# Kernel tuning notes

Measured on AMD Instinct MI355X. Metric: run time of the kernel, lower is better.

The kernel has to match this reference:

```python
import jax, jax.numpy as jnp
import numpy as np

EPS = 1e-5  # BatchNorm eps
N_NODES, N_EDGES, F = 100000, 600000, 128


def setup_inputs() -> dict:
    key = jax.random.key(0)
    ks = jax.random.split(key, 16)
    inp = {
        "node_representations": jax.random.normal(ks[0], (N_NODES, F), jnp.float32),
        "edges": jax.random.randint(ks[1], (2, N_EDGES), 0, N_NODES, jnp.int64 if jax.config.jax_enable_x64 else jnp.int32),
        "edge_weights": jax.random.uniform(ks[2], (N_EDGES,), jnp.float32),
        # preprocess FFN: BatchNorm1d(F) [eval mode] + Linear(F, F) + GELU
        "pre_bn_gamma": jax.random.normal(ks[3], (F,), jnp.float32) * 0.1 + 1.0,
        "pre_bn_beta": jax.random.normal(ks[4], (F,), jnp.float32) * 0.1,
        "pre_bn_mean": jax.random.normal(ks[5], (F,), jnp.float32) * 0.1,
        "pre_bn_var": jax.random.uniform(ks[6], (F,), jnp.float32) * 0.5 + 0.5,
        "pre_w": jax.random.normal(ks[7], (F, F), jnp.float32) / np.sqrt(F),
        "pre_b": jnp.zeros((F,), jnp.float32),
        # update FFN: BatchNorm1d(2F) [eval mode] + Linear(2F, F) + GELU
        "upd_bn_gamma": jax.random.normal(ks[8], (2 * F,), jnp.float32) * 0.1 + 1.0,
        "upd_bn_beta": jax.random.normal(ks[9], (2 * F,), jnp.float32) * 0.1,
        "upd_bn_mean": jax.random.normal(ks[10], (2 * F,), jnp.float32) * 0.1,
        "upd_bn_var": jax.random.uniform(ks[11], (2 * F,), jnp.float32) * 0.5 + 0.5,
        "upd_w": jax.random.normal(ks[12], (2 * F, F), jnp.float32) / np.sqrt(2 * F),
        "upd_b": jnp.zeros((F,), jnp.float32),
    }
    return inp


def _bn_eval(x, gamma, beta, mean, var):
    return (x - mean) * (gamma / jnp.sqrt(var + EPS)) + beta


def reference(node_representations, edges, edge_weights,
              pre_bn_gamma, pre_bn_beta, pre_bn_mean, pre_bn_var, pre_w, pre_b,
              upd_bn_gamma, upd_bn_beta, upd_bn_mean, upd_bn_var, upd_w, upd_b):
    n_nodes, f = node_representations.shape
    node_idx, nbr_idx = edges[0], edges[1]
    # gather neighbour features: [E, F]
    x = node_representations[nbr_idx]
    # preprocess FFN (BN eval, dropout=identity in eval, linear, gelu)
    x = _bn_eval(x, pre_bn_gamma, pre_bn_beta, pre_bn_mean, pre_bn_var)
    x = jax.nn.gelu(x @ pre_w + pre_b, approximate=False)
    x = x * edge_weights[:, None]
    # mean aggregation (replicates torch.unique-on-expanded-indices counter = degree * F)
    agg = jax.ops.segment_sum(x, node_idx, num_segments=n_nodes)
    deg = jax.ops.segment_sum(jnp.ones_like(edge_weights), node_idx, num_segments=n_nodes)
    counter = (deg * f)[:, None]
    agg = jnp.where(counter > 0, agg / jnp.where(counter > 0, counter, 1.0), 0.0)
    # concat combine + update FFN
    emb = jnp.concatenate([node_representations, agg], axis=-1)
    emb = _bn_eval(emb, upd_bn_gamma, upd_bn_beta, upd_bn_mean, upd_bn_var)
    emb = jax.nn.gelu(emb @ upd_w + upd_b, approximate=False)
    return emb
```

## Files before the change

### kernel.cpp

```cpp
#include <hip/hip_runtime.h>
#include <math.h>

#define F 128
#define TWO_F 256
#define BN_EPS 1e-5f
#define PAD_W1 136
#define PAD_W2 264

typedef unsigned short ushort_t;
typedef unsigned char uchar_t;
typedef __attribute__((ext_vector_type(8))) short bfrag;
typedef __attribute__((ext_vector_type(4))) float ffrag;
typedef __attribute__((ext_vector_type(2))) float floatx2;

__device__ __forceinline__ float gelu_exact(float x) {
    return 0.5f * x * (1.0f + erff(x * 0.70710678118654752f));
}
__device__ __forceinline__ ushort_t f2bf(float x) {
    unsigned int u = __float_as_uint(x);
    u = (u + 0x7FFFu + ((u >> 16) & 1u)) >> 16;
    return (ushort_t)u;
}
__device__ __forceinline__ unsigned int pk2(float a, float b) {
    return (unsigned int)f2bf(a) | ((unsigned int)f2bf(b) << 16);
}

__device__ __forceinline__ void fma4_fp8(float* acc, unsigned int d, float w) {
    floatx2 lo = __builtin_amdgcn_cvt_pk_f32_fp8(d, false);
    floatx2 hi = __builtin_amdgcn_cvt_pk_f32_fp8(d, true);
    acc[0] = fmaf(w, lo.x, acc[0]);
    acc[1] = fmaf(w, lo.y, acc[1]);
    acc[2] = fmaf(w, hi.x, acc[2]);
    acc[3] = fmaf(w, hi.y, acc[3]);
}
__device__ __forceinline__ void fma16_fp8(float* acc, uint4 a, float w) {
    fma4_fp8(acc + 0,  a.x, w); fma4_fp8(acc + 4,  a.y, w);
    fma4_fp8(acc + 8,  a.z, w); fma4_fp8(acc + 12, a.w, w);
}

__global__ __launch_bounds__(256) void prep(
    const float* __restrict__ pre_w, const float* __restrict__ pre_b,
    const float* __restrict__ g1, const float* __restrict__ be1,
    const float* __restrict__ m1, const float* __restrict__ v1,
    const float* __restrict__ upd_w, const float* __restrict__ upd_b,
    const float* __restrict__ g2, const float* __restrict__ be2,
    const float* __restrict__ m2, const float* __restrict__ v2,
    ushort_t* __restrict__ W1T, ushort_t* __restrict__ W2T,
    float* __restrict__ b1f, float* __restrict__ b2f,
    const float* __restrict__ nodes, ushort_t* __restrict__ NB, int convB, int nNodes,
    const int* __restrict__ edges, int* __restrict__ counts, int* __restrict__ rankb,
    int nEdges, int histBlocks) {
    const int t = threadIdx.x;
    if (blockIdx.x == 0) {
        __shared__ float t1[F], t2[TWO_F];
        if (t < F) {
            float s = g1[t] * rsqrtf(v1[t] + BN_EPS);
            t1[t] = be1[t] - m1[t] * s;
        }
        {
            float s = g2[t] * rsqrtf(v2[t] + BN_EPS);
            t2[t] = be2[t] - m2[t] * s;
        }
        __syncthreads();
        if (t < F) {
            float acc = pre_b[t];
            #pragma unroll 4
            for (int k = 0; k < F; ++k) acc = fmaf(t1[k], pre_w[k * F + t], acc);
            b1f[t] = acc;
        } else {
            int j = t - F;
            float acc = upd_b[j];
            #pragma unroll 4
            for (int k = 0; k < TWO_F; ++k) acc = fmaf(t2[k], upd_w[k * F + j], acc);
            b2f[j] = acc;
        }
    } else if (blockIdx.x <= 128) {
        int idx = (blockIdx.x - 1) * 256 + t;
        if (idx < F * F) {
            int k = idx & (F - 1), n = idx >> 7;
            float s = g1[k] * rsqrtf(v1[k] + BN_EPS);
            W1T[idx] = f2bf(s * pre_w[k * F + n]);
        }
        {
            int k = idx & (TWO_F - 1), n = idx >> 8;
            float s = g2[k] * rsqrtf(v2[k] + BN_EPS);
            W2T[idx] = f2bf(s * upd_w[k * F + n]);
        }
    } else if (blockIdx.x <= 128 + convB) {
        int cb = blockIdx.x - 129;
        long long idx = (long long)cb * 4096 + t * 16;
        if (idx < (long long)nNodes * F) {
            const float4* s = reinterpret_cast<const float4*>(nodes + idx);
            float4 f0 = s[0], f1 = s[1], f2 = s[2], f3 = s[3];
            uint4 o0, o1;
            o0.x = pk2(f0.x, f0.y); o0.y = pk2(f0.z, f0.w);
            o0.z = pk2(f1.x, f1.y); o0.w = pk2(f1.z, f1.w);
            o1.x = pk2(f2.x, f2.y); o1.y = pk2(f2.z, f2.w);
            o1.z = pk2(f3.x, f3.y); o1.w = pk2(f3.z, f3.w);
            uint4* d = reinterpret_cast<uint4*>(NB + idx);
            d[0] = o0; d[1] = o1;
        }
    } else {
        int b = blockIdx.x - 129 - convB;
        for (int i = b * 256 + t; i < nEdges; i += histBlocks * 256) {
            int rk = atomicAdd(&counts[edges[i]], 1);
            rankb[i] = rk;
        }
    }
}

__global__ __launch_bounds__(1024) void scan_pass1(const int* __restrict__ counts,
                                                   int* __restrict__ offsets,
                                                   int* __restrict__ blocksums, int n) {
    __shared__ int sb[1024];
    const int t = threadIdx.x;
    int idx = blockIdx.x * 1024 + t;
    int v = (idx < n) ? counts[idx] : 0;
    sb[t] = v;
    __syncthreads();
    for (int off = 1; off < 1024; off <<= 1) {
        int x = (t >= off) ? sb[t - off] : 0;
        __syncthreads();
        sb[t] += x;
        __syncthreads();
    }
    if (idx < n) offsets[idx + 1] = sb[t];
    if (t == 1023) blocksums[blockIdx.x] = sb[t];
}

__global__ __launch_bounds__(1024) void scan_pass3(const int* __restrict__ counts,
                                                   int* __restrict__ offsets,
                                                   const int* __restrict__ blocksums,
                                                   int* __restrict__ cursor, int n) {
    __shared__ int sb[1024];
    const int t = threadIdx.x;
    sb[t] = (t < blockIdx.x) ? blocksums[t] : 0;
    __syncthreads();
    #pragma unroll
    for (int off = 512; off > 0; off >>= 1) {
        if (t < off) sb[t] += sb[t + off];
        __syncthreads();
    }
    int base = sb[0];
    int idx = blockIdx.x * 1024 + t;
    if (idx < n) {
        int incl = offsets[idx + 1] + base;
        offsets[idx + 1] = incl;
        cursor[idx] = incl - counts[idx];
    }
    if (blockIdx.x == 0 && t == 0) offsets[0] = 0;
}

__global__ __launch_bounds__(256) void gemm1_fill(
    const ushort_t* __restrict__ NB, const ushort_t* __restrict__ W1T,
    const float* __restrict__ b1f, uchar_t* __restrict__ G8, int nNodes,
    const int* __restrict__ edges, const float* __restrict__ ew,
    const int* __restrict__ offsets, const int* __restrict__ rankb,
    int2* __restrict__ csr, int nEdges,
    int gemmBlocks, int fillBlocks, int nTiles) {
    __shared__ ushort_t Wl[F * PAD_W1];
    __shared__ float bsm[F];
    __shared__ uchar_t bounce[4][16 * F];
    const int t = threadIdx.x;

    if (blockIdx.x >= gemmBlocks) {
        int b = blockIdx.x - gemmBlocks;
        for (int e = b * 256 + t; e < nEdges; e += fillBlocks * 256) {
            int dst = edges[e];
            int pos = offsets[dst] + rankb[e];
            csr[pos] = make_int2(edges[nEdges + e], __float_as_int(ew[e]));
        }
        return;
    }

    for (int j = t; j < 2048; j += 256) {
        int feat = j >> 4, kc = j & 15;
        *reinterpret_cast<uint4*>(Wl + feat * PAD_W1 + kc * 8) =
            reinterpret_cast<const uint4*>(W1T)[j];
    }
    if (t < F) bsm[t] = b1f[t];
    __syncthreads();

    const int lane = t & 63, w = t >> 6;
    const int m = lane & 15, quad = lane >> 4;
    const int rr = lane >> 2, cc = (lane & 3) * 32;

    for (int tile = blockIdx.x; tile < nTiles; tile += gemmBlocks) {
        const int tb = tile * 64;
        int arow = tb + w * 16 + m;
        if (arow >= nNodes) arow = 0;
        const ushort_t* ap = NB + (size_t)arow * F + quad * 8;

        bfrag a[4];
        #pragma unroll
        for (int kk = 0; kk < 4; ++kk)
            a[kk] = *reinterpret_cast<const bfrag*>(ap + kk * 32);

        ffrag acc[8];
        #pragma unroll
        for (int c = 0; c < 8; ++c) acc[c] = (ffrag){0.f, 0.f, 0.f, 0.f};

        #pragma unroll
        for (int kk = 0; kk < 4; ++kk) {
            int k0 = kk * 32 + quad * 8;
            #pragma unroll
            for (int c = 0; c < 8; ++c) {
                bfrag b = *reinterpret_cast<const bfrag*>(Wl + (c * 16 + m) * PAD_W1 + k0);
                acc[c] = __builtin_amdgcn_mfma_f32_16x16x32_bf16(a[kk], b, acc[c], 0, 0, 0);
            }
        }

        #pragma unroll
        for (int c = 0; c < 8; ++c) {
            float bj = bsm[c * 16 + m];
            #pragma unroll
            for (int i = 0; i < 4; ++i) {
                float v = gelu_exact(acc[c][i] + bj);
                int pkd = __builtin_amdgcn_cvt_pk_fp8_f32(v, v, 0, false);
                bounce[w][(quad * 4 + i) * F + c * 16 + m] = (uchar_t)(pkd & 0xFF);
            }
        }
        uint4 d0 = *reinterpret_cast<const uint4*>(&bounce[w][rr * F + cc]);
        uint4 d1 = *reinterpret_cast<const uint4*>(&bounce[w][rr * F + cc + 16]);
        int gr = tb + w * 16 + rr;
        if (gr < nNodes) {
            *reinterpret_cast<uint4*>(G8 + (size_t)gr * F + cc) = d0;
            *reinterpret_cast<uint4*>(G8 + (size_t)gr * F + cc + 16) = d1;
        }
    }
}

__global__ __launch_bounds__(256) void gather_agg(
    const uchar_t* __restrict__ G8, const int* __restrict__ offsets,
    const int2* __restrict__ csr, ushort_t* __restrict__ agg, int nNodes) {
    const int t = threadIdx.x;
    const int gid = blockIdx.x * 32 + (t >> 3);
    const int q = t & 7;
    if (gid >= nNodes) return;
    const int s = offsets[gid], e = offsets[gid + 1];

    float acc[16];
    #pragma unroll
    for (int j = 0; j < 16; ++j) acc[j] = 0.f;

    int i = s;
    while (i < e) {
        int c = e - i;
        c = (c > 8) ? 8 : c;
        uint4 av[8];
        float wv[8];
        #pragma unroll
        for (int j = 0; j < 8; ++j) {
            if (j < c) {
                int2 m = csr[i + j];
                wv[j] = __int_as_float(m.y);
                av[j] = *reinterpret_cast<const uint4*>(
                    G8 + (size_t)(unsigned int)m.x * F + q * 16);
            }
        }
        #pragma unroll
        for (int j = 0; j < 8; ++j)
            if (j < c) fma16_fp8(acc, av[j], wv[j]);
        i += c;
    }

    const int deg = e - s;
    const float inv = (deg > 0) ? 1.0f / ((float)deg * (float)F) : 0.f;
    uint4 pv0, pv1;
    pv0.x = pk2(acc[0] * inv, acc[1] * inv);  pv0.y = pk2(acc[2] * inv, acc[3] * inv);
    pv0.z = pk2(acc[4] * inv, acc[5] * inv);  pv0.w = pk2(acc[6] * inv, acc[7] * inv);
    pv1.x = pk2(acc[8] * inv, acc[9] * inv);  pv1.y = pk2(acc[10] * inv, acc[11] * inv);
    pv1.z = pk2(acc[12] * inv, acc[13] * inv); pv1.w = pk2(acc[14] * inv, acc[15] * inv);
    uint4* d = reinterpret_cast<uint4*>(agg + (size_t)gid * F + q * 16);
    d[0] = pv0; d[1] = pv1;
}

__global__ __launch_bounds__(512, 4) void gemm2(
    const ushort_t* __restrict__ NB, const ushort_t* __restrict__ agg,
    const ushort_t* __restrict__ W2T, const float* __restrict__ b2f,
    float* __restrict__ out, int nNodes) {
    __shared__ ushort_t Wl[F * PAD_W2];
    __shared__ float bsm[F];
    const int t = threadIdx.x;

    for (int j = t; j < 4096; j += 512) {
        int feat = j >> 5, kc = j & 31;
        *reinterpret_cast<uint4*>(Wl + feat * PAD_W2 + kc * 8) =
            reinterpret_cast<const uint4*>(W2T)[j];
    }
    if (t < F) bsm[t] = b2f[t];
    __syncthreads();

    const int lane = t & 63, w = t >> 6;
    const int m = lane & 15, quad = lane >> 4;
    const int tb = blockIdx.x * 256;

    int row0 = tb + w * 32 + m;
    int row1 = row0 + 16;
    int r0c = (row0 < nNodes) ? row0 : 0;
    int r1c = (row1 < nNodes) ? row1 : 0;
    const ushort_t* p0n = NB  + (size_t)r0c * F + quad * 8;
    const ushort_t* p1n = NB  + (size_t)r1c * F + quad * 8;
    const ushort_t* p0a = agg + (size_t)r0c * F + quad * 8;
    const ushort_t* p1a = agg + (size_t)r1c * F + quad * 8;

    ffrag acc0[8], acc1[8];
    #pragma unroll
    for (int c = 0; c < 8; ++c) {
        acc0[c] = (ffrag){0.f, 0.f, 0.f, 0.f};
        acc1[c] = (ffrag){0.f, 0.f, 0.f, 0.f};
    }

    #pragma unroll
    for (int kk = 0; kk < 8; ++kk) {
        int k0 = kk * 32 + quad * 8;
        bfrag a0 = (kk < 4)
            ? *reinterpret_cast<const bfrag*>(p0n + kk * 32)
            : *reinterpret_cast<const bfrag*>(p0a + (kk - 4) * 32);
        bfrag a1 = (kk < 4)
            ? *reinterpret_cast<const bfrag*>(p1n + kk * 32)
            : *reinterpret_cast<const bfrag*>(p1a + (kk - 4) * 32);
        #pragma unroll
        for (int c = 0; c < 8; ++c) {
            bfrag b = *reinterpret_cast<const bfrag*>(Wl + (c * 16 + m) * PAD_W2 + k0);
            acc0[c] = __builtin_amdgcn_mfma_f32_16x16x32_bf16(a0, b, acc0[c], 0, 0, 0);
            acc1[c] = __builtin_amdgcn_mfma_f32_16x16x32_bf16(a1, b, acc1[c], 0, 0, 0);
        }
    }

    #pragma unroll
    for (int c = 0; c < 8; ++c) {
        int feat = c * 16 + m;
        float bj = bsm[feat];
        #pragma unroll
        for (int i = 0; i < 4; ++i) {
            int n0 = tb + w * 32 + quad * 4 + i;
            if (n0 < nNodes) out[(size_t)n0 * F + feat] = gelu_exact(acc0[c][i] + bj);
            int n1 = n0 + 16;
            if (n1 < nNodes) out[(size_t)n1 * F + feat] = gelu_exact(acc1[c][i] + bj);
        }
    }
}

extern "C" void kernel_launch(void* const* d_in, const int* in_sizes, int n_in,
                              void* d_out, int out_size, void* d_ws, size_t ws_size,
                              hipStream_t stream) {
    const float* nodes  = (const float*)d_in[0];
    const int*   edges  = (const int*)d_in[1];
    const float* ew     = (const float*)d_in[2];
    const float* pre_g  = (const float*)d_in[3];
    const float* pre_be = (const float*)d_in[4];
    const float* pre_m  = (const float*)d_in[5];
    const float* pre_v  = (const float*)d_in[6];
    const float* pre_w  = (const float*)d_in[7];
    const float* pre_b  = (const float*)d_in[8];
    const float* upd_g  = (const float*)d_in[9];
    const float* upd_be = (const float*)d_in[10];
    const float* upd_m  = (const float*)d_in[11];
    const float* upd_v  = (const float*)d_in[12];
    const float* upd_w  = (const float*)d_in[13];
    const float* upd_b  = (const float*)d_in[14];
    float* out = (float*)d_out;

    const int nNodes = in_sizes[0] / F;
    const int nEdges = in_sizes[2];
    const int nChunks = (nNodes + 1023) / 1024;
    const int histBlocks = 1024;
    const int convB = (int)(((long long)nNodes * F + 4095) / 4096);
    const int gemmBlocks = 768;
    const int fillBlocks = 512;
    const int nTiles = (nNodes + 63) / 64;

    char* p = (char*)d_ws;
    int*      counts    = (int*)p;       p += (size_t)nNodes * 4;
    int*      offsets   = (int*)p;       p += (size_t)(nNodes + 4) * 4;
    int*      cursor    = (int*)p;       p += (size_t)nNodes * 4;
    int*      blocksums = (int*)p;       p += 1024 * 4;
    int2*     csr       = (int2*)p;      p += (size_t)nEdges * 8;
    float*    b1f       = (float*)p;     p += F * 4;
    float*    b2f       = (float*)p;     p += F * 4;
    ushort_t* W1T       = (ushort_t*)p;  p += F * F * 2;
    ushort_t* W2T       = (ushort_t*)p;  p += TWO_F * F * 2;
    uchar_t*  G8        = (uchar_t*)p;   p += (size_t)nNodes * F;
    ushort_t* agg       = (ushort_t*)p;  p += (size_t)nNodes * F * 2;
    int*      rankb     = (int*)p;       p += (size_t)nEdges * 4;
    ushort_t* NB        = (ushort_t*)p;

    hipMemsetAsync(counts, 0, (size_t)nNodes * 4, stream);

    prep<<<129 + convB + histBlocks, 256, 0, stream>>>(
        pre_w, pre_b, pre_g, pre_be, pre_m, pre_v,
        upd_w, upd_b, upd_g, upd_be, upd_m, upd_v,
        W1T, W2T, b1f, b2f, nodes, NB, convB, nNodes,
        edges, counts, rankb, nEdges, histBlocks);

    scan_pass1<<<nChunks, 1024, 0, stream>>>(counts, offsets, blocksums, nNodes);
    scan_pass3<<<nChunks, 1024, 0, stream>>>(counts, offsets, blocksums, cursor, nNodes);

    gemm1_fill<<<gemmBlocks + fillBlocks, 256, 0, stream>>>(
        NB, W1T, b1f, G8, nNodes, edges, ew, offsets, rankb, csr, nEdges,
        gemmBlocks, fillBlocks, nTiles);

    gather_agg<<<(nNodes + 31) / 32, 256, 0, stream>>>(
        G8, offsets, csr, agg, nNodes);

    gemm2<<<(nNodes + 255) / 256, 512, 0, stream>>>(
        NB, agg, W2T, b2f, out, nNodes);
}
```

Before: 267.8 us.

## Fuse fp32-to-bf16 node conversion into GEMM loads and split prep kernel

```diff
diff --git a/kernel.cpp b/kernel.cpp
--- a/kernel.cpp
+++ b/kernel.cpp
@@ -38,7 +38,15 @@
     fma4_fp8(acc + 8,  a.z, w); fma4_fp8(acc + 12, a.w, w);
 }
 
-__global__ __launch_bounds__(256) void prep(
+__device__ __forceinline__ bfrag pack8(float4 f0, float4 f1) {
+    bfrag a;
+    unsigned int* au = reinterpret_cast<unsigned int*>(&a);
+    au[0] = pk2(f0.x, f0.y); au[1] = pk2(f0.z, f0.w);
+    au[2] = pk2(f1.x, f1.y); au[3] = pk2(f1.z, f1.w);
+    return a;
+}
+
+__global__ __launch_bounds__(256) void fold(
     const float* __restrict__ pre_w, const float* __restrict__ pre_b,
     const float* __restrict__ g1, const float* __restrict__ be1,
     const float* __restrict__ m1, const float* __restrict__ v1,
@@ -46,10 +54,7 @@
     const float* __restrict__ g2, const float* __restrict__ be2,
     const float* __restrict__ m2, const float* __restrict__ v2,
     ushort_t* __restrict__ W1T, ushort_t* __restrict__ W2T,
-    float* __restrict__ b1f, float* __restrict__ b2f,
-    const float* __restrict__ nodes, ushort_t* __restrict__ NB, int convB, int nNodes,
-    const int* __restrict__ edges, int* __restrict__ counts, int* __restrict__ rankb,
-    int nEdges, int histBlocks) {
+    float* __restrict__ b1f, float* __restrict__ b2f) {
     const int t = threadIdx.x;
     if (blockIdx.x == 0) {
         __shared__ float t1[F], t2[TWO_F];
@@ -64,17 +69,17 @@
         __syncthreads();
         if (t < F) {
             float acc = pre_b[t];
-            #pragma unroll 4
+            #pragma unroll 16
             for (int k = 0; k < F; ++k) acc = fmaf(t1[k], pre_w[k * F + t], acc);
             b1f[t] = acc;
         } else {
             int j = t - F;
             float acc = upd_b[j];
-            #pragma unroll 4
+            #pragma unroll 16
             for (int k = 0; k < TWO_F; ++k) acc = fmaf(t2[k], upd_w[k * F + j], acc);
             b2f[j] = acc;
         }
-    } else if (blockIdx.x <= 128) {
+    } else {
         int idx = (blockIdx.x - 1) * 256 + t;
         if (idx < F * F) {
             int k = idx & (F - 1), n = idx >> 7;
@@ -86,26 +91,16 @@
             float s = g2[k] * rsqrtf(v2[k] + BN_EPS);
             W2T[idx] = f2bf(s * upd_w[k * F + n]);
         }
-    } else if (blockIdx.x <= 128 + convB) {
-        int cb = blockIdx.x - 129;
-        long long idx = (long long)cb * 4096 + t * 16;
-        if (idx < (long long)nNodes * F) {
-            const float4* s = reinterpret_cast<const float4*>(nodes + idx);
-            float4 f0 = s[0], f1 = s[1], f2 = s[2], f3 = s[3];
-            uint4 o0, o1;
-            o0.x = pk2(f0.x, f0.y); o0.y = pk2(f0.z, f0.w);
-            o0.z = pk2(f1.x, f1.y); o0.w = pk2(f1.z, f1.w);
-            o1.x = pk2(f2.x, f2.y); o1.y = pk2(f2.z, f2.w);
-            o1.z = pk2(f3.x, f3.y); o1.w = pk2(f3.z, f3.w);
-            uint4* d = reinterpret_cast<uint4*>(NB + idx);
-            d[0] = o0; d[1] = o1;
-        }
-    } else {
-        int b = blockIdx.x - 129 - convB;
-        for (int i = b * 256 + t; i < nEdges; i += histBlocks * 256) {
-            int rk = atomicAdd(&counts[edges[i]], 1);
-            rankb[i] = rk;
-        }
+    }
+}
+
+__global__ __launch_bounds__(256) void hist(
+    const int* __restrict__ edges, int* __restrict__ counts,
+    int* __restrict__ rankb, int nEdges) {
+    const int stride = gridDim.x * 256;
+    for (int i = blockIdx.x * 256 + threadIdx.x; i < nEdges; i += stride) {
+        int rk = atomicAdd(&counts[edges[i]], 1);
+        rankb[i] = rk;
     }
 }
 
@@ -152,7 +147,7 @@
 }
 
 __global__ __launch_bounds__(256) void gemm1_fill(
-    const ushort_t* __restrict__ NB, const ushort_t* __restrict__ W1T,
+    const float* __restrict__ nodes, const ushort_t* __restrict__ W1T,
     const float* __restrict__ b1f, uchar_t* __restrict__ G8, int nNodes,
     const int* __restrict__ edges, const float* __restrict__ ew,
     const int* __restrict__ offsets, const int* __restrict__ rankb,
@@ -189,12 +184,15 @@
         const int tb = tile * 64;
         int arow = tb + w * 16 + m;
         if (arow >= nNodes) arow = 0;
-        const ushort_t* ap = NB + (size_t)arow * F + quad * 8;
+        const float* ap = nodes + (size_t)arow * F + quad * 8;
 
         bfrag a[4];
         #pragma unroll
-        for (int kk = 0; kk < 4; ++kk)
-            a[kk] = *reinterpret_cast<const bfrag*>(ap + kk * 32);
+        for (int kk = 0; kk < 4; ++kk) {
+            float4 f0 = *reinterpret_cast<const float4*>(ap + kk * 32);
+            float4 f1 = *reinterpret_cast<const float4*>(ap + kk * 32 + 4);
+            a[kk] = pack8(f0, f1);
+        }
 
         ffrag acc[8];
         #pragma unroll
@@ -276,7 +274,7 @@
 }
 
 __global__ __launch_bounds__(512, 4) void gemm2(
-    const ushort_t* __restrict__ NB, const ushort_t* __restrict__ agg,
+    const float* __restrict__ nodes, const ushort_t* __restrict__ agg,
     const ushort_t* __restrict__ W2T, const float* __restrict__ b2f,
     float* __restrict__ out, int nNodes) {
     __shared__ ushort_t Wl[F * PAD_W2];
@@ -299,10 +297,10 @@
     int row1 = row0 + 16;
     int r0c = (row0 < nNodes) ? row0 : 0;
     int r1c = (row1 < nNodes) ? row1 : 0;
-    const ushort_t* p0n = NB  + (size_t)r0c * F + quad * 8;
-    const ushort_t* p1n = NB  + (size_t)r1c * F + quad * 8;
-    const ushort_t* p0a = agg + (size_t)r0c * F + quad * 8;
-    const ushort_t* p1a = agg + (size_t)r1c * F + quad * 8;
+    const float*    p0n = nodes + (size_t)r0c * F + quad * 8;
+    const float*    p1n = nodes + (size_t)r1c * F + quad * 8;
+    const ushort_t* p0a = agg   + (size_t)r0c * F + quad * 8;
+    const ushort_t* p1a = agg   + (size_t)r1c * F + quad * 8;
 
     ffrag acc0[8], acc1[8];
     #pragma unroll
@@ -314,12 +312,18 @@
     #pragma unroll
     for (int kk = 0; kk < 8; ++kk) {
         int k0 = kk * 32 + quad * 8;
-        bfrag a0 = (kk < 4)
-            ? *reinterpret_cast<const bfrag*>(p0n + kk * 32)
-            : *reinterpret_cast<const bfrag*>(p0a + (kk - 4) * 32);
-        bfrag a1 = (kk < 4)
-            ? *reinterpret_cast<const bfrag*>(p1n + kk * 32)
-            : *reinterpret_cast<const bfrag*>(p1a + (kk - 4) * 32);
+        bfrag a0, a1;
+        if (kk < 4) {
+            float4 f0 = *reinterpret_cast<const float4*>(p0n + kk * 32);
+            float4 f1 = *reinterpret_cast<const float4*>(p0n + kk * 32 + 4);
+            a0 = pack8(f0, f1);
+            float4 g0 = *reinterpret_cast<const float4*>(p1n + kk * 32);
+            float4 g1 = *reinterpret_cast<const float4*>(p1n + kk * 32 + 4);
+            a1 = pack8(g0, g1);
+        } else {
+            a0 = *reinterpret_cast<const bfrag*>(p0a + (kk - 4) * 32);
+            a1 = *reinterpret_cast<const bfrag*>(p1a + (kk - 4) * 32);
+        }
         #pragma unroll
         for (int c = 0; c < 8; ++c) {
             bfrag b = *reinterpret_cast<const bfrag*>(Wl + (c * 16 + m) * PAD_W2 + k0);
@@ -366,7 +370,6 @@
     const int nEdges = in_sizes[2];
     const int nChunks = (nNodes + 1023) / 1024;
     const int histBlocks = 1024;
-    const int convB = (int)(((long long)nNodes * F + 4095) / 4096);
     const int gemmBlocks = 768;
     const int fillBlocks = 512;
     const int nTiles = (nNodes + 63) / 64;
@@ -383,27 +386,27 @@
     ushort_t* W2T       = (ushort_t*)p;  p += TWO_F * F * 2;
     uchar_t*  G8        = (uchar_t*)p;   p += (size_t)nNodes * F;
     ushort_t* agg       = (ushort_t*)p;  p += (size_t)nNodes * F * 2;
-    int*      rankb     = (int*)p;       p += (size_t)nEdges * 4;
-    ushort_t* NB        = (ushort_t*)p;
+    int*      rankb     = (int*)p;
 
     hipMemsetAsync(counts, 0, (size_t)nNodes * 4, stream);
 
-    prep<<<129 + convB + histBlocks, 256, 0, stream>>>(
+    fold<<<129, 256, 0, stream>>>(
         pre_w, pre_b, pre_g, pre_be, pre_m, pre_v,
         upd_w, upd_b, upd_g, upd_be, upd_m, upd_v,
-        W1T, W2T, b1f, b2f, nodes, NB, convB, nNodes,
-        edges, counts, rankb, nEdges, histBlocks);
+        W1T, W2T, b1f, b2f);
+
+    hist<<<histBlocks, 256, 0, stream>>>(edges, counts, rankb, nEdges);
 
     scan_pass1<<<nChunks, 1024, 0, stream>>>(counts, offsets, blocksums, nNodes);
     scan_pass3<<<nChunks, 1024, 0, stream>>>(counts, offsets, blocksums, cursor, nNodes);
 
     gemm1_fill<<<gemmBlocks + fillBlocks, 256, 0, stream>>>(
-        NB, W1T, b1f, G8, nNodes, edges, ew, offsets, rankb, csr, nEdges,
+        nodes, W1T, b1f, G8, nNodes, edges, ew, offsets, rankb, csr, nEdges,
         gemmBlocks, fillBlocks, nTiles);
 
     gather_agg<<<(nNodes + 31) / 32, 256, 0, stream>>>(
         G8, offsets, csr, agg, nNodes);
 
     gemm2<<<(nNodes + 255) / 256, 512, 0, stream>>>(
-        NB, agg, W2T, b2f, out, nNodes);
-}
+        nodes, agg, W2T, b2f, out, nNodes);
+}
```

New measurement: 254.4 us. -5.0%, faster.
